# Performance work log

Measured on AMD Instinct MI355X. Metric: run time of the kernel, lower is better.

Reference implementation:

```python
import jax, jax.numpy as jnp
import numpy as np


def setup_inputs() -> dict:
    key = jax.random.key(0)
    ks = jax.random.split(key, 12)
    N, D = 150000, 100          # user_num + news_num nodes, emb_dim
    T, E, S = 16, 262144, 4096  # timesteps, edges/step, seeds/step
    CAT, K = 20, 9
    return {
        "node_emb": jax.random.normal(ks[0], (N, D), jnp.float32),
        "cx": jax.random.normal(ks[1], (N, D), jnp.float32),
        "rel_emb": jax.random.normal(ks[2], (CAT, D), jnp.float32),
        "W_ih": jax.random.normal(ks[3], (4 * D, D), jnp.float32) * 0.1,
        "W_hh": jax.random.normal(ks[4], (4 * D, D), jnp.float32) * 0.1,
        "b_ih": jax.random.normal(ks[5], (4 * D,), jnp.float32) * 0.1,
        "b_hh": jax.random.normal(ks[6], (4 * D,), jnp.float32) * 0.1,
        "src": jax.random.randint(ks[7], (T, E), 0, N, jnp.int64),
        "dst": jax.random.randint(ks[8], (T, E), 0, N, jnp.int64),
        "cat": jax.random.randint(ks[9], (T, E), 0, CAT, jnp.int64),
        "seeds": jax.random.randint(ks[10], (T, S), 0, 100000, jnp.int64),
        "cand_idx": jax.random.randint(ks[11], (T * S, K), 0, N, jnp.int64),
    }


def reference(node_emb, cx, rel_emb, W_ih, W_hh, b_ih, b_hh,
              src, dst, cat, seeds, cand_idx):
    N, D = node_emb.shape

    def step(carry, inputs):
        emb, c = carry
        s, d, ct, seed = inputs
        # previous hidden/cell state of seed users (before aggregation)
        h_prev = emb[seed]            # [S, D]
        c_prev = c[seed]              # [S, D]
        # edge-weighted gather-multiply-mean aggregation (send_and_recv)
        msg = emb[s] * rel_emb[ct]    # [E, D]
        agg = jax.ops.segment_sum(msg, d, num_segments=N)          # [N, D]
        cnt = jax.ops.segment_sum(jnp.ones(d.shape, emb.dtype), d,
                                  num_segments=N)                  # [N]
        emb = emb + agg / jnp.maximum(cnt, 1.0)[:, None]           # residual add
        # LSTMCell update on seed users
        x = emb[seed]                                              # [S, D]
        gates = x @ W_ih.T + b_ih + h_prev @ W_hh.T + b_hh         # [S, 4D]
        i_g, f_g, g_g, o_g = jnp.split(gates, 4, axis=-1)
        c_new = jax.nn.sigmoid(f_g) * c_prev + jax.nn.sigmoid(i_g) * jnp.tanh(g_g)
        h_new = jax.nn.sigmoid(o_g) * jnp.tanh(c_new)
        emb = emb.at[seed].set(h_new)
        c = c.at[seed].set(c_new)
        return (emb, c), h_new

    (emb_final, _), seed_embs = jax.lax.scan(
        step, (node_emb, cx), (src, dst, cat, seeds))
    # seed_embs: [T, S, D] -> per-click user embeddings
    user = seed_embs.reshape(-1, D)           # [T*S, D]
    cand = emb_final[cand_idx]                # [T*S, K, D]
    scores = jnp.einsum('nd,nkd->nk', user, cand)
    return scores
```

## Files before the change

kernel.cpp:

```cpp
#include <hip/hip_runtime.h>
#include <math.h>

#define N_NODES 150000
#define NODE_STRIDE 150016
#define DIM 100
#define D4 25
#define T_STEPS 16
#define E_EDGES 262144
#define S_SEEDS 4096
#define K_CAND 9
#define SPB 8
#define NPB 8

#define CB 32
#define BSPAN 4688

__device__ __forceinline__ float sigmoidf_(float x) {
    return 1.0f / (1.0f + __expf(-x));
}


__global__ __launch_bounds__(256) void coarse_hist(
    const int* __restrict__ dst, int* __restrict__ ccnt) {
    int t = blockIdx.x >> 10;
    int i = blockIdx.x * 256 + threadIdx.x;
    __shared__ int h[CB];
    if (threadIdx.x < CB) h[threadIdx.x] = 0;
    __syncthreads();
    int d = dst[i];
    atomicAdd(&h[d / BSPAN], 1);
    __syncthreads();
    if (threadIdx.x < CB)
        atomicAdd(&ccnt[t * CB + threadIdx.x], h[threadIdx.x]);
}

__global__ __launch_bounds__(64) void coarse_scan(
    const int* __restrict__ ccnt, int* __restrict__ coffs,
    int* __restrict__ ccur) {
    int t = blockIdx.x;
    int tid = threadIdx.x;
    __shared__ int sh[CB];
    if (tid < CB) sh[tid] = ccnt[t * CB + tid];
    __syncthreads();
    if (tid == 0) {
        int run = 0;
        for (int b = 0; b < CB; b++) { int c = sh[b]; sh[b] = run; run += c; }
    }
    __syncthreads();
    if (tid < CB) {
        coffs[t * (CB + 1) + tid] = sh[tid];
        ccur[t * CB + tid] = sh[tid];
    }
    if (tid == 0) coffs[t * (CB + 1) + CB] = E_EDGES;
}

__global__ __launch_bounds__(256) void coarse_scatter(
    const int* __restrict__ src, const int* __restrict__ dst,
    const int* __restrict__ cat, int* __restrict__ ccur,
    int2* __restrict__ cbuf) {
    int t = blockIdx.x >> 10;
    int i = blockIdx.x * 256 + threadIdx.x;
    __shared__ int h[CB];
    __shared__ int base[CB];
    if (threadIdx.x < CB) h[threadIdx.x] = 0;
    __syncthreads();
    int d = dst[i];
    int b = d / BSPAN;
    int rank = atomicAdd(&h[b], 1);
    __syncthreads();
    if (threadIdx.x < CB && h[threadIdx.x] > 0)
        base[threadIdx.x] = atomicAdd(&ccur[t * CB + threadIdx.x], h[threadIdx.x]);
    __syncthreads();
    int2 entry;
    entry.x = src[i] | (cat[i] << 18);
    entry.y = d;
    cbuf[(size_t)t * E_EDGES + base[b] + rank] = entry;
}

__global__ __launch_bounds__(256) void fine_build(
    const int2* __restrict__ cbuf, const int* __restrict__ coffs,
    int* __restrict__ offs, int* __restrict__ sorted) {
    int t = blockIdx.x >> 5;
    int b = blockIdx.x & 31;
    int node0 = b * BSPAN;
    int nodes = min(BSPAN, N_NODES - node0);
    int ebeg = coffs[t * (CB + 1) + b];
    int eend = coffs[t * (CB + 1) + b + 1];
    const int2* ebuf = cbuf + (size_t)t * E_EDGES;
    int* off = offs + (size_t)t * NODE_STRIDE;
    int* srt = sorted + (size_t)t * E_EDGES;
    __shared__ int cnt[BSPAN];
    __shared__ int sums[256];
    int tid = threadIdx.x;

    for (int j = tid; j < BSPAN; j += 256) cnt[j] = 0;
    __syncthreads();
    for (int e = ebeg + tid; e < eend; e += 256)
        atomicAdd(&cnt[ebuf[e].y - node0], 1);
    __syncthreads();

    const int chunk = (BSPAN + 255) / 256;
    int cbeg = tid * chunk;
    int cend = min(cbeg + chunk, BSPAN);
    int s = 0;
    for (int j = cbeg; j < cend; j++) s += cnt[j];
    sums[tid] = s;
    __syncthreads();
    for (int d = 1; d < 256; d <<= 1) {
        int v = (tid >= d) ? sums[tid - d] : 0;
        __syncthreads();
        sums[tid] += v;
        __syncthreads();
    }
    int run = (tid == 0) ? 0 : sums[tid - 1];
    for (int j = cbeg; j < cend; j++) {
        int c = cnt[j];
        cnt[j] = run;
        if (j < nodes) off[node0 + j] = ebeg + run;
        run += c;
    }
    if (tid == 0 && b == CB - 1) off[N_NODES] = E_EDGES;
    __syncthreads();

    for (int e = ebeg + tid; e < eend; e += 256) {
        int2 en = ebuf[e];
        int pos = atomicAdd(&cnt[en.y - node0], 1);
        srt[ebeg + pos] = en.x;
    }
}

__global__ __launch_bounds__(256) void fused_agg(
    const float* __restrict__ emb_in, float* __restrict__ emb_out,
    const float* __restrict__ rel_emb, const int* __restrict__ offs,
    const int* __restrict__ sorted) {
    int g = threadIdx.x >> 5;
    int lane = threadIdx.x & 31;
    int node = blockIdx.x * NPB + g;
    if (node >= N_NODES) return;
    int beg = offs[node], end = offs[node + 1];
    bool act = lane < D4;
    float4 acc = make_float4(0.f, 0.f, 0.f, 0.f);
    int e = beg;
    for (; e + 1 < end; e += 2) {
        int p0 = sorted[e], p1 = sorted[e + 1];
        int s0 = p0 & 0x3FFFF, c0 = p0 >> 18;
        int s1 = p1 & 0x3FFFF, c1 = p1 >> 18;
        if (act) {
            float4 m0 = ((const float4*)(emb_in + (size_t)s0 * DIM))[lane];
            float4 r0 = ((const float4*)(rel_emb + (size_t)c0 * DIM))[lane];
            float4 m1 = ((const float4*)(emb_in + (size_t)s1 * DIM))[lane];
            float4 r1 = ((const float4*)(rel_emb + (size_t)c1 * DIM))[lane];
            acc.x += m0.x * r0.x; acc.y += m0.y * r0.y;
            acc.z += m0.z * r0.z; acc.w += m0.w * r0.w;
            acc.x += m1.x * r1.x; acc.y += m1.y * r1.y;
            acc.z += m1.z * r1.z; acc.w += m1.w * r1.w;
        }
    }
    if (e < end) {
        int p = sorted[e];
        int s = p & 0x3FFFF, c = p >> 18;
        if (act) {
            float4 m = ((const float4*)(emb_in + (size_t)s * DIM))[lane];
            float4 r = ((const float4*)(rel_emb + (size_t)c * DIM))[lane];
            acc.x += m.x * r.x; acc.y += m.y * r.y;
            acc.z += m.z * r.z; acc.w += m.w * r.w;
        }
    }
    if (act) {
        float4 bv = ((const float4*)(emb_in + (size_t)node * DIM))[lane];
        float inv = (end > beg) ? 1.0f / (float)(end - beg) : 0.0f;
        bv.x += acc.x * inv; bv.y += acc.y * inv;
        bv.z += acc.z * inv; bv.w += acc.w * inv;
        ((float4*)(emb_out + (size_t)node * DIM))[lane] = bv;
    }
}

__global__ __launch_bounds__(512) void lstm_kernel(
    const float* __restrict__ emb_new, const float* __restrict__ emb_old,
    const float* __restrict__ c_state, const int* __restrict__ seeds,
    const float* __restrict__ W_ih, const float* __restrict__ W_hh,
    const float* __restrict__ b_ih, const float* __restrict__ b_hh,
    float* __restrict__ h_out, float* __restrict__ c_out) {
    __shared__ float xs[SPB][DIM];
    __shared__ float hs[SPB][DIM];
    __shared__ float gates[SPB][4 * DIM];
    int tid = threadIdx.x;
    int base = blockIdx.x * SPB;

    for (int idx = tid; idx < SPB * DIM; idx += 512) {
        int s = idx / DIM, d = idx - s * DIM;
        int node = seeds[base + s];
        xs[s][d] = emb_new[(size_t)node * DIM + d];
        hs[s][d] = emb_old[(size_t)node * DIM + d];
    }
    __syncthreads();

    if (tid < 4 * DIM) {
        int j = tid;
        float acc[SPB];
#pragma unroll
        for (int s = 0; s < SPB; s++) acc[s] = 0.0f;
        const float* wi = W_ih + (size_t)j * DIM;
        const float* wh = W_hh + (size_t)j * DIM;
        for (int d = 0; d < DIM; d++) {
            float a = wi[d], b = wh[d];
#pragma unroll
            for (int s = 0; s < SPB; s++)
                acc[s] += xs[s][d] * a + hs[s][d] * b;
        }
        float bb = b_ih[j] + b_hh[j];
#pragma unroll
        for (int s = 0; s < SPB; s++) gates[s][j] = acc[s] + bb;
    }
    __syncthreads();

    for (int idx = tid; idx < SPB * DIM; idx += 512) {
        int s = idx / DIM, d = idx - s * DIM;
        int node = seeds[base + s];
        float ig = gates[s][d];
        float fg = gates[s][DIM + d];
        float gg = gates[s][2 * DIM + d];
        float og = gates[s][3 * DIM + d];
        float cp = c_state[(size_t)node * DIM + d];
        float cn = sigmoidf_(fg) * cp + sigmoidf_(ig) * tanhf(gg);
        float hn = sigmoidf_(og) * tanhf(cn);
        h_out[(size_t)(base + s) * DIM + d] = hn;
        c_out[(size_t)(base + s) * DIM + d] = cn;
    }
}

__global__ __launch_bounds__(256) void scatter_seed(
    float* __restrict__ emb, float* __restrict__ c_state,
    const int* __restrict__ seeds,
    const float* __restrict__ h_new, const float* __restrict__ c_new) {
    int i = blockIdx.x * blockDim.x + threadIdx.x;
    int sd = i / D4, q = i - sd * D4;
    int node = seeds[sd];
    ((float4*)(emb + (size_t)node * DIM))[q] = ((const float4*)h_new)[i];
    ((float4*)(c_state + (size_t)node * DIM))[q] = ((const float4*)c_new)[i];
}

__global__ __launch_bounds__(64) void score_kernel(
    const float* __restrict__ seed_h, const float* __restrict__ emb,
    const int* __restrict__ cand_idx, float* __restrict__ out) {
    int n = blockIdx.x;
    int lane = threadIdx.x;
    float u0 = seed_h[(size_t)n * DIM + lane];
    float u1 = (lane + 64 < DIM) ? seed_h[(size_t)n * DIM + lane + 64] : 0.0f;
    for (int k = 0; k < K_CAND; k++) {
        int node = cand_idx[n * K_CAND + k];
        const float* ce = emb + (size_t)node * DIM;
        float p = u0 * ce[lane];
        if (lane + 64 < DIM) p += u1 * ce[lane + 64];
        for (int off = 32; off > 0; off >>= 1) p += __shfl_down(p, off);
        if (lane == 0) out[n * K_CAND + k] = p;
    }
}

extern "C" void kernel_launch(void* const* d_in, const int* in_sizes, int n_in,
                              void* d_out, int out_size, void* d_ws, size_t ws_size,
                              hipStream_t stream) {
    const float* node_emb = (const float*)d_in[0];
    const float* cx       = (const float*)d_in[1];
    const float* rel_emb  = (const float*)d_in[2];
    const float* W_ih     = (const float*)d_in[3];
    const float* W_hh     = (const float*)d_in[4];
    const float* b_ih     = (const float*)d_in[5];
    const float* b_hh     = (const float*)d_in[6];
    const int*   src      = (const int*)d_in[7];
    const int*   dst      = (const int*)d_in[8];
    const int*   cat      = (const int*)d_in[9];
    const int*   seeds    = (const int*)d_in[10];
    const int*   cand     = (const int*)d_in[11];
    float* out = (float*)d_out;

    float* ws = (float*)d_ws;
    float* emb_a = ws; ws += (size_t)N_NODES * DIM;
    float* emb_b = ws; ws += (size_t)N_NODES * DIM;
    float* cst   = ws; ws += (size_t)N_NODES * DIM;
    float* cnew  = ws; ws += (size_t)S_SEEDS * DIM;
    float* seedh = ws; ws += (size_t)T_STEPS * S_SEEDS * DIM;
    int* offs    = (int*)ws; ws += (size_t)T_STEPS * NODE_STRIDE;
    int* sorted  = (int*)ws; ws += (size_t)T_STEPS * E_EDGES;
    int* ccnt    = (int*)ws; ws += T_STEPS * CB;
    int* ccur    = (int*)ws; ws += T_STEPS * CB;
    int* coffs   = (int*)ws; ws += T_STEPS * (CB + 1);
    int2* cbuf = (int2*)emb_b;

    hipMemsetAsync(ccnt, 0, sizeof(int) * T_STEPS * CB, stream);
    coarse_hist<<<T_STEPS * 1024, 256, 0, stream>>>(dst, ccnt);
    coarse_scan<<<T_STEPS, 64, 0, stream>>>(ccnt, coffs, ccur);
    coarse_scatter<<<T_STEPS * 1024, 256, 0, stream>>>(src, dst, cat, ccur, cbuf);
    fine_build<<<T_STEPS * CB, 256, 0, stream>>>(cbuf, coffs, offs, sorted);

    hipMemcpyAsync(emb_a, node_emb, sizeof(float) * (size_t)N_NODES * DIM,
                   hipMemcpyDeviceToDevice, stream);
    hipMemcpyAsync(cst, cx, sizeof(float) * (size_t)N_NODES * DIM,
                   hipMemcpyDeviceToDevice, stream);

    float* cur = emb_a;
    float* nxt = emb_b;
    for (int t = 0; t < T_STEPS; t++) {
        fused_agg<<<(N_NODES + NPB - 1) / NPB, 256, 0, stream>>>(
            cur, nxt, rel_emb,
            offs + (size_t)t * NODE_STRIDE, sorted + (size_t)t * E_EDGES);
        lstm_kernel<<<S_SEEDS / SPB, 512, 0, stream>>>(
            nxt, cur, cst, seeds + (size_t)t * S_SEEDS,
            W_ih, W_hh, b_ih, b_hh,
            seedh + (size_t)t * S_SEEDS * DIM, cnew);
        scatter_seed<<<(S_SEEDS * D4) / 256, 256, 0, stream>>>(
            nxt, cst, seeds + (size_t)t * S_SEEDS,
            seedh + (size_t)t * S_SEEDS * DIM, cnew);
        float* tmp = cur; cur = nxt; nxt = tmp;
    }
    score_kernel<<<T_STEPS * S_SEEDS, 64, 0, stream>>>(seedh, cur, cand, out);
}
```

Baseline: 1.843 ms.

## Pack per-node degree and first edges into int4 meta, vectorize LSTM matvec

```diff
diff --git a/kernel.cpp b/kernel.cpp
--- a/kernel.cpp
+++ b/kernel.cpp
@@ -9,7 +9,7 @@
 #define E_EDGES 262144
 #define S_SEEDS 4096
 #define K_CAND 9
-#define SPB 8
+#define SPB 16
 #define NPB 8
 
 #define CB 32
@@ -79,7 +79,7 @@
 
 __global__ __launch_bounds__(256) void fine_build(
     const int2* __restrict__ cbuf, const int* __restrict__ coffs,
-    int* __restrict__ offs, int* __restrict__ sorted) {
+    int4* __restrict__ meta, int* __restrict__ sorted) {
     int t = blockIdx.x >> 5;
     int b = blockIdx.x & 31;
     int node0 = b * BSPAN;
@@ -87,9 +87,10 @@
     int ebeg = coffs[t * (CB + 1) + b];
     int eend = coffs[t * (CB + 1) + b + 1];
     const int2* ebuf = cbuf + (size_t)t * E_EDGES;
-    int* off = offs + (size_t)t * NODE_STRIDE;
+    int4* mt = meta + (size_t)t * NODE_STRIDE;
     int* srt = sorted + (size_t)t * E_EDGES;
     __shared__ int cnt[BSPAN];
+    __shared__ int begs[BSPAN];
     __shared__ int sums[256];
     int tid = threadIdx.x;
 
@@ -115,11 +116,10 @@
     int run = (tid == 0) ? 0 : sums[tid - 1];
     for (int j = cbeg; j < cend; j++) {
         int c = cnt[j];
+        begs[j] = run;
         cnt[j] = run;
-        if (j < nodes) off[node0 + j] = ebeg + run;
         run += c;
     }
-    if (tid == 0 && b == CB - 1) off[N_NODES] = E_EDGES;
     __syncthreads();
 
     for (int e = ebeg + tid; e < eend; e += 256) {
@@ -127,51 +127,64 @@
         int pos = atomicAdd(&cnt[en.y - node0], 1);
         srt[ebeg + pos] = en.x;
     }
+    __syncthreads();
+
+    for (int j = tid; j < nodes; j += 256) {
+        int lbeg = begs[j];
+        int deg = cnt[j] - lbeg;
+        int gbeg = ebeg + lbeg;
+        int4 m;
+        m.x = deg;
+        m.y = gbeg;
+        m.z = (deg > 0) ? srt[gbeg] : 0;
+        m.w = (deg > 1) ? srt[gbeg + 1] : 0;
+        mt[node0 + j] = m;
+    }
 }
 
 __global__ __launch_bounds__(256) void fused_agg(
     const float* __restrict__ emb_in, float* __restrict__ emb_out,
-    const float* __restrict__ rel_emb, const int* __restrict__ offs,
+    const float* __restrict__ rel_emb, const int4* __restrict__ meta,
     const int* __restrict__ sorted) {
     int g = threadIdx.x >> 5;
     int lane = threadIdx.x & 31;
     int node = blockIdx.x * NPB + g;
     if (node >= N_NODES) return;
-    int beg = offs[node], end = offs[node + 1];
     bool act = lane < D4;
+    int4 m = meta[node];
+    int deg = m.x;
+    float4 own = act ? ((const float4*)(emb_in + (size_t)node * DIM))[lane]
+                     : make_float4(0.f, 0.f, 0.f, 0.f);
     float4 acc = make_float4(0.f, 0.f, 0.f, 0.f);
-    int e = beg;
-    for (; e + 1 < end; e += 2) {
-        int p0 = sorted[e], p1 = sorted[e + 1];
-        int s0 = p0 & 0x3FFFF, c0 = p0 >> 18;
-        int s1 = p1 & 0x3FFFF, c1 = p1 >> 18;
-        if (act) {
-            float4 m0 = ((const float4*)(emb_in + (size_t)s0 * DIM))[lane];
-            float4 r0 = ((const float4*)(rel_emb + (size_t)c0 * DIM))[lane];
-            float4 m1 = ((const float4*)(emb_in + (size_t)s1 * DIM))[lane];
-            float4 r1 = ((const float4*)(rel_emb + (size_t)c1 * DIM))[lane];
-            acc.x += m0.x * r0.x; acc.y += m0.y * r0.y;
-            acc.z += m0.z * r0.z; acc.w += m0.w * r0.w;
+    if (deg > 0 && act) {
+        float4 m0 = ((const float4*)(emb_in + (size_t)(m.z & 0x3FFFF) * DIM))[lane];
+        float4 r0 = ((const float4*)(rel_emb + (size_t)(m.z >> 18) * DIM))[lane];
+        float4 m1, r1;
+        if (deg > 1) {
+            m1 = ((const float4*)(emb_in + (size_t)(m.w & 0x3FFFF) * DIM))[lane];
+            r1 = ((const float4*)(rel_emb + (size_t)(m.w >> 18) * DIM))[lane];
+        }
+        acc.x += m0.x * r0.x; acc.y += m0.y * r0.y;
+        acc.z += m0.z * r0.z; acc.w += m0.w * r0.w;
+        if (deg > 1) {
             acc.x += m1.x * r1.x; acc.y += m1.y * r1.y;
             acc.z += m1.z * r1.z; acc.w += m1.w * r1.w;
         }
     }
-    if (e < end) {
+    for (int e = m.y + 2; e < m.y + deg; e++) {
         int p = sorted[e];
-        int s = p & 0x3FFFF, c = p >> 18;
         if (act) {
-            float4 m = ((const float4*)(emb_in + (size_t)s * DIM))[lane];
-            float4 r = ((const float4*)(rel_emb + (size_t)c * DIM))[lane];
-            acc.x += m.x * r.x; acc.y += m.y * r.y;
-            acc.z += m.z * r.z; acc.w += m.w * r.w;
+            float4 mm = ((const float4*)(emb_in + (size_t)(p & 0x3FFFF) * DIM))[lane];
+            float4 rr = ((const float4*)(rel_emb + (size_t)(p >> 18) * DIM))[lane];
+            acc.x += mm.x * rr.x; acc.y += mm.y * rr.y;
+            acc.z += mm.z * rr.z; acc.w += mm.w * rr.w;
         }
     }
     if (act) {
-        float4 bv = ((const float4*)(emb_in + (size_t)node * DIM))[lane];
-        float inv = (end > beg) ? 1.0f / (float)(end - beg) : 0.0f;
-        bv.x += acc.x * inv; bv.y += acc.y * inv;
-        bv.z += acc.z * inv; bv.w += acc.w * inv;
-        ((float4*)(emb_out + (size_t)node * DIM))[lane] = bv;
+        float inv = (deg > 0) ? 1.0f / (float)deg : 0.0f;
+        own.x += acc.x * inv; own.y += acc.y * inv;
+        own.z += acc.z * inv; own.w += acc.w * inv;
+        ((float4*)(emb_out + (size_t)node * DIM))[lane] = own;
     }
 }
 
@@ -181,8 +194,8 @@
     const float* __restrict__ W_ih, const float* __restrict__ W_hh,
     const float* __restrict__ b_ih, const float* __restrict__ b_hh,
     float* __restrict__ h_out, float* __restrict__ c_out) {
-    __shared__ float xs[SPB][DIM];
-    __shared__ float hs[SPB][DIM];
+    __shared__ __align__(16) float xs[SPB][DIM];
+    __shared__ __align__(16) float hs[SPB][DIM];
     __shared__ float gates[SPB][4 * DIM];
     int tid = threadIdx.x;
     int base = blockIdx.x * SPB;
@@ -200,13 +213,17 @@
         float acc[SPB];
 #pragma unroll
         for (int s = 0; s < SPB; s++) acc[s] = 0.0f;
-        const float* wi = W_ih + (size_t)j * DIM;
-        const float* wh = W_hh + (size_t)j * DIM;
-        for (int d = 0; d < DIM; d++) {
-            float a = wi[d], b = wh[d];
+        const float4* wi = (const float4*)(W_ih + (size_t)j * DIM);
+        const float4* wh = (const float4*)(W_hh + (size_t)j * DIM);
+        for (int dc = 0; dc < D4; dc++) {
+            float4 a = wi[dc], b = wh[dc];
 #pragma unroll
-            for (int s = 0; s < SPB; s++)
-                acc[s] += xs[s][d] * a + hs[s][d] * b;
+            for (int s = 0; s < SPB; s++) {
+                float4 x = ((const float4*)xs[s])[dc];
+                float4 h = ((const float4*)hs[s])[dc];
+                acc[s] += x.x * a.x + x.y * a.y + x.z * a.z + x.w * a.w
+                        + h.x * b.x + h.y * b.y + h.z * b.z + h.w * b.w;
+            }
         }
         float bb = b_ih[j] + b_hh[j];
 #pragma unroll
@@ -236,8 +253,10 @@
     int i = blockIdx.x * blockDim.x + threadIdx.x;
     int sd = i / D4, q = i - sd * D4;
     int node = seeds[sd];
-    ((float4*)(emb + (size_t)node * DIM))[q] = ((const float4*)h_new)[i];
-    ((float4*)(c_state + (size_t)node * DIM))[q] = ((const float4*)c_new)[i];
+    ((float4*)(emb + (size_t)node * DIM))[q] =
+        ((const float4*)(h_new + (size_t)sd * DIM))[q];
+    ((float4*)(c_state + (size_t)node * DIM))[q] =
+        ((const float4*)(c_new + (size_t)sd * DIM))[q];
 }
 
 __global__ __launch_bounds__(64) void score_kernel(
@@ -274,24 +293,24 @@
     const int*   cand     = (const int*)d_in[11];
     float* out = (float*)d_out;
 
-    float* ws = (float*)d_ws;
-    float* emb_a = ws; ws += (size_t)N_NODES * DIM;
-    float* emb_b = ws; ws += (size_t)N_NODES * DIM;
-    float* cst   = ws; ws += (size_t)N_NODES * DIM;
-    float* cnew  = ws; ws += (size_t)S_SEEDS * DIM;
-    float* seedh = ws; ws += (size_t)T_STEPS * S_SEEDS * DIM;
-    int* offs    = (int*)ws; ws += (size_t)T_STEPS * NODE_STRIDE;
-    int* sorted  = (int*)ws; ws += (size_t)T_STEPS * E_EDGES;
-    int* ccnt    = (int*)ws; ws += T_STEPS * CB;
-    int* ccur    = (int*)ws; ws += T_STEPS * CB;
-    int* coffs   = (int*)ws; ws += T_STEPS * (CB + 1);
+    char* wsb = (char*)d_ws;
+    float* emb_a = (float*)wsb; wsb += sizeof(float) * (size_t)N_NODES * DIM;
+    float* emb_b = (float*)wsb; wsb += sizeof(float) * (size_t)N_NODES * DIM;
+    float* cst   = (float*)wsb; wsb += sizeof(float) * (size_t)N_NODES * DIM;
+    float* cnew  = (float*)wsb; wsb += sizeof(float) * (size_t)S_SEEDS * DIM;
+    float* seedh = (float*)wsb; wsb += sizeof(float) * (size_t)T_STEPS * S_SEEDS * DIM;
+    int4* meta   = (int4*)wsb; wsb += sizeof(int4) * (size_t)T_STEPS * NODE_STRIDE;
+    int* sorted  = (int*)wsb; wsb += sizeof(int) * (size_t)T_STEPS * E_EDGES;
+    int* ccnt    = (int*)wsb; wsb += sizeof(int) * T_STEPS * CB;
+    int* ccur    = (int*)wsb; wsb += sizeof(int) * T_STEPS * CB;
+    int* coffs   = (int*)wsb; wsb += sizeof(int) * T_STEPS * (CB + 1);
     int2* cbuf = (int2*)emb_b;
 
     hipMemsetAsync(ccnt, 0, sizeof(int) * T_STEPS * CB, stream);
     coarse_hist<<<T_STEPS * 1024, 256, 0, stream>>>(dst, ccnt);
     coarse_scan<<<T_STEPS, 64, 0, stream>>>(ccnt, coffs, ccur);
     coarse_scatter<<<T_STEPS * 1024, 256, 0, stream>>>(src, dst, cat, ccur, cbuf);
-    fine_build<<<T_STEPS * CB, 256, 0, stream>>>(cbuf, coffs, offs, sorted);
+    fine_build<<<T_STEPS * CB, 256, 0, stream>>>(cbuf, coffs, meta, sorted);
 
     hipMemcpyAsync(emb_a, node_emb, sizeof(float) * (size_t)N_NODES * DIM,
                    hipMemcpyDeviceToDevice, stream);
@@ -303,7 +322,7 @@
     for (int t = 0; t < T_STEPS; t++) {
         fused_agg<<<(N_NODES + NPB - 1) / NPB, 256, 0, stream>>>(
             cur, nxt, rel_emb,
-            offs + (size_t)t * NODE_STRIDE, sorted + (size_t)t * E_EDGES);
+            meta + (size_t)t * NODE_STRIDE, sorted + (size_t)t * E_EDGES);
         lstm_kernel<<<S_SEEDS / SPB, 512, 0, stream>>>(
             nxt, cur, cst, seeds + (size_t)t * S_SEEDS,
             W_ih, W_hh, b_ih, b_hh,
```

Result: faster. 1.690 ms (-8.3%).
